# Kernel tuning notes

Measured on AMD Instinct MI355X. Metric: run time of the kernel, lower is better.

## Reference

```python
import jax, jax.numpy as jnp
import numpy as np

V, K, E, H, B, T = 30000, 9, 300, 300, 64, 512


def _lstm_dir(pre, W_hh, reverse):
    # pre: [T, B, 4H] = x @ W_ih.T + b_ih + b_hh, torch gate order (i, f, g, o)
    Bsz = pre.shape[1]
    Hh = W_hh.shape[1]
    h0 = jnp.zeros((Bsz, Hh), pre.dtype)
    c0 = jnp.zeros((Bsz, Hh), pre.dtype)

    def step(carry, p):
        h, c = carry
        gates = p + h @ W_hh.T
        i, f, g, o = jnp.split(gates, 4, axis=-1)
        i = jax.nn.sigmoid(i)
        f = jax.nn.sigmoid(f)
        o = jax.nn.sigmoid(o)
        g = jnp.tanh(g)
        c = f * c + i * g
        h = o * jnp.tanh(c)
        return (h, c), h

    _, hs = jax.lax.scan(step, (h0, c0), pre, reverse=reverse)
    return hs  # [T, B, H], time-aligned with input (reverse dir handled by scan)


def _crf_loglik(em, tags, mask, start, end, trans):
    # torchcrf CRF log-likelihood, reduction='sum'. em: [B,T,K], mask: [B,T] float.
    em_sc = jnp.take_along_axis(em, tags[..., None], axis=-1)[..., 0]  # [B,T]
    tr_sc = trans[tags[:, :-1], tags[:, 1:]]                            # [B,T-1]
    seq_len = jnp.sum(mask, axis=1).astype(jnp.int32)                   # [B]
    last_tags = jnp.take_along_axis(tags, (seq_len - 1)[:, None], axis=1)[:, 0]
    num = start[tags[:, 0]] + em_sc[:, 0]
    num = num + jnp.sum((tr_sc + em_sc[:, 1:]) * mask[:, 1:], axis=1)
    num = num + end[last_tags]

    # forward algorithm (partition function)
    alpha0 = start[None, :] + em[:, 0]             # [B,K]
    em_t = jnp.swapaxes(em[:, 1:], 0, 1)           # [T-1,B,K]
    m_t = jnp.swapaxes(mask[:, 1:], 0, 1)          # [T-1,B]

    def step(alpha, xs):
        e, m = xs
        nxt = jax.nn.logsumexp(alpha[:, :, None] + trans[None] + e[:, None, :], axis=1)
        return jnp.where(m[:, None] > 0, nxt, alpha), None

    alpha, _ = jax.lax.scan(step, alpha0, (em_t, m_t))
    den = jax.nn.logsumexp(alpha + end[None, :], axis=1)
    return jnp.sum(num - den)


def _forward(x, y, embedding, W_ih_f, W_hh_f, b_ih_f, b_hh_f,
             W_ih_b, W_hh_b, b_ih_b, b_hh_b, W_lin, b_lin,
             start_trans, end_trans, trans):
    emb = embedding[x]                       # [B,T,E]
    emb_t = jnp.swapaxes(emb, 0, 1)          # [T,B,E]
    pre_f = emb_t @ W_ih_f.T + (b_ih_f + b_hh_f)
    pre_b = emb_t @ W_ih_b.T + (b_ih_b + b_hh_b)
    hs_f = _lstm_dir(pre_f, W_hh_f, reverse=False)
    hs_b = _lstm_dir(pre_b, W_hh_b, reverse=True)
    out = jnp.concatenate([hs_f, hs_b], axis=-1)  # [T,B,2H]
    out = jnp.swapaxes(out, 0, 1)                 # [B,T,2H]
    logits = out @ W_lin.T + b_lin
    probs = jax.nn.softmax(logits, axis=-1)
    mask = (y != -1).astype(probs.dtype)
    llh = _crf_loglik(probs, y, mask, start_trans, end_trans, trans)
    return probs, -llh


def setup_inputs() -> dict:
    key = jax.random.key(0)
    ks = jax.random.split(key, 17)

    def p(k, shape, s=0.05):
        return jax.random.normal(k, shape, dtype=jnp.float32) * s

    return {
        "x": jax.random.randint(ks[0], (B, T), 0, V),
        "y": jax.random.randint(ks[1], (B, T), 0, K),
        "embedding": p(ks[2], (V, E), 1.0),
        "W_ih_f": p(ks[3], (4 * H, E)),
        "W_hh_f": p(ks[4], (4 * H, H)),
        "b_ih_f": p(ks[5], (4 * H,)),
        "b_hh_f": p(ks[6], (4 * H,)),
        "W_ih_b": p(ks[7], (4 * H, E)),
        "W_hh_b": p(ks[8], (4 * H, H)),
        "b_ih_b": p(ks[9], (4 * H,)),
        "b_hh_b": p(ks[10], (4 * H,)),
        "W_lin": p(ks[11], (K, 2 * H)),
        "b_lin": p(ks[12], (K,)),
        "start_trans": p(ks[13], (K,), 0.1),
        "end_trans": p(ks[14], (K,), 0.1),
        "trans": p(ks[15], (K, K), 0.1),
    }


def reference(x, y, embedding, W_ih_f, W_hh_f, b_ih_f, b_hh_f,
              W_ih_b, W_hh_b, b_ih_b, b_hh_b, W_lin, b_lin,
              start_trans, end_trans, trans):
    return _forward(x, y, embedding, W_ih_f, W_hh_f, b_ih_f, b_hh_f,
                    W_ih_b, W_hh_b, b_ih_b, b_hh_b, W_lin, b_lin,
                    start_trans, end_trans, trans)
```

## Files before the change

kernel.cpp:

```cpp
#include <hip/hip_runtime.h>
#include <stdint.h>

#define TSEQ 512
#define NB   64
#define EMB  300
#define HID  300
#define G4   1200
#define KKP  150
#define NT   9
#define MTOT (TSEQ*NB)

#define NP 19
#define NQ 4
#define NWG (2*NQ*NP)
#define KSTEPS 10
#define HROWS 160

typedef _Float16 h2v __attribute__((ext_vector_type(2)));
typedef _Float16 f16x8 __attribute__((ext_vector_type(8)));
typedef float f32x4 __attribute__((ext_vector_type(4)));
union H2U { uint32_t u; h2v h; };

__device__ __forceinline__ uint32_t packf2(float a, float b) {
  H2U u; u.h.x = (_Float16)a; u.h.y = (_Float16)b; return u.u;
}

__device__ __forceinline__ float sigm(float x) { return 1.0f / (1.0f + expf(-x)); }

__global__ __launch_bounds__(256) void prep_wih(
    const float* __restrict__ Wihf, const float* __restrict__ Wihb,
    uint32_t* __restrict__ wtih) {
  int i = blockIdx.x * 256 + threadIdx.x;
  if (i >= KKP * G4) return;
  int m = blockIdx.y;
  int kk = i / G4, g = i % G4;
  const float* src = (m == 0) ? Wihf : Wihb;
  float2 v = *(const float2*)(src + (size_t)g * 300 + 2 * kk);
  wtih[(size_t)m * (KKP * G4) + i] = packf2(v.x, v.y);
}

__global__ __launch_bounds__(256) void prep_bias(
    const float* __restrict__ bihf, const float* __restrict__ bhhf,
    const float* __restrict__ bihb, const float* __restrict__ bhhb,
    float* __restrict__ bias) {
  int i = blockIdx.x * 256 + threadIdx.x;
  if (i < G4) {
    bias[i]       = bihf[i] + bhhf[i];
    bias[G4 + i]  = bihb[i] + bhhb[i];
  }
}

__global__ __launch_bounds__(64) void prep_w3(
    const float* __restrict__ Whhf, const float* __restrict__ Whhb,
    uint32_t* __restrict__ w2) {
  int blk = blockIdx.x;
  int ks = blk % KSTEPS; int tmp = blk / KSTEPS;
  int w = tmp & 3; tmp >>= 2;
  int p = tmp % NP; int d = tmp / NP;
  int lane = threadIdx.x;
  const float* W = d ? Whhb : Whhf;
  int m = lane & 15;
  int gamma = m >> 2, rr = m & 3;
  int hid = 16 * p + 4 * w + rr;
  int k0 = ks * 32 + (lane >> 4) * 8;
  float vals[8];
  #pragma unroll
  for (int e = 0; e < 8; ++e) {
    int k = k0 + e;
    vals[e] = (hid < 300 && k < 300) ? W[(size_t)(gamma * 300 + hid) * 300 + k] : 0.0f;
  }
  uint4 dw;
  dw.x = packf2(vals[0], vals[1]);
  dw.y = packf2(vals[2], vals[3]);
  dw.z = packf2(vals[4], vals[5]);
  dw.w = packf2(vals[6], vals[7]);
  *(uint4*)(w2 + ((size_t)blk * 64 + lane) * 4) = dw;
}

__global__ __launch_bounds__(256) void init_sync(
    uint32_t* __restrict__ flags, uint32_t* __restrict__ h2g) {
  int i = blockIdx.x * 256 + threadIdx.x;
  if (i < 8 * 128) flags[i] = 0;
  if (i < 2 * 2 * HROWS * 64) h2g[i] = 0;
}

__global__ __launch_bounds__(256) void gather_emb(
    const int* __restrict__ x, const float* __restrict__ emb,
    uint32_t* __restrict__ Ae) {
  __shared__ __align__(16) uint32_t buf[64 * KKP];
  __shared__ int idxs[64];
  int tid = threadIdx.x;
  int m0 = blockIdx.x * 64;
  if (tid < 64) {
    int mm = m0 + tid;
    idxs[tid] = x[(size_t)(mm & 63) * TSEQ + (mm >> 6)];
  }
  __syncthreads();
  for (int i = tid; i < 64 * KKP; i += 256) {
    int mm = i / KKP, kk = i % KKP;
    float2 v = *(const float2*)(emb + (size_t)idxs[mm] * EMB + 2 * kk);
    buf[i] = packf2(v.x, v.y);
  }
  __syncthreads();
  for (int i = tid; i < 64 * KKP; i += 256) {
    int kk = i >> 6, mm = i & 63;
    Ae[(size_t)kk * MTOT + m0 + mm] = buf[mm * KKP + kk];
  }
}

__global__ __launch_bounds__(256) void embed_pre_mfma(
    const uint32_t* __restrict__ Ae, const uint32_t* __restrict__ wtih,
    const float* __restrict__ bias, _Float16* __restrict__ pre) {
  const int d = blockIdx.z;
  const int tid = threadIdx.x;
  const int w = tid >> 6, lane = tid & 63;
  const int n0 = blockIdx.x * 64 + w * 16;
  const int m00 = blockIdx.y * 128;
  const int col = n0 + (lane & 15);
  const bool colok = col < G4;
  const int rsel = lane >> 4;
  const uint32_t* Wd = wtih + (size_t)d * (KKP * G4);
  uint32_t bfr[KSTEPS][4];
  #pragma unroll
  for (int ks = 0; ks < KSTEPS; ++ks)
    #pragma unroll
    for (int j = 0; j < 4; ++j) {
      int kk = ks * 16 + rsel * 4 + j;
      bfr[ks][j] = (kk < KKP && colok) ? Wd[(size_t)kk * G4 + col] : 0u;
    }
  float bcol = colok ? bias[d * G4 + col] : 0.0f;
  for (int mb = 0; mb < 8; ++mb) {
    const int m0 = m00 + mb * 16;
    uint32_t afr[KSTEPS][4];
    #pragma unroll
    for (int ks = 0; ks < KSTEPS; ++ks)
      #pragma unroll
      for (int j = 0; j < 4; ++j) {
        int kk = ks * 16 + rsel * 4 + j;
        afr[ks][j] = (kk < KKP) ? Ae[(size_t)kk * MTOT + m0 + (lane & 15)] : 0u;
      }
    f32x4 acc; acc[0] = bcol; acc[1] = bcol; acc[2] = bcol; acc[3] = bcol;
    #pragma unroll
    for (int ks = 0; ks < KSTEPS; ++ks) {
      union { uint32_t u[4]; f16x8 v; } au, bu;
      au.u[0] = afr[ks][0]; au.u[1] = afr[ks][1]; au.u[2] = afr[ks][2]; au.u[3] = afr[ks][3];
      bu.u[0] = bfr[ks][0]; bu.u[1] = bfr[ks][1]; bu.u[2] = bfr[ks][2]; bu.u[3] = bfr[ks][3];
      acc = __builtin_amdgcn_mfma_f32_16x16x32_f16(au.v, bu.v, acc, 0, 0, 0);
    }
    if (colok) {
      #pragma unroll
      for (int j = 0; j < 4; ++j) {
        int m = m0 + rsel * 4 + j;
        pre[((size_t)d * MTOT + m) * G4 + col] = (_Float16)acc[j];
      }
    }
  }
}

__global__ __launch_bounds__(256) void lstm_mfma(
    const uint32_t* __restrict__ w2, const _Float16* __restrict__ pre,
    uint32_t* __restrict__ h2g, uint32_t* __restrict__ hs16,
    uint32_t* __restrict__ flags) {
  const int wg = blockIdx.x;
  const int p  = wg % NP;
  const int dq = wg / NP;
  const int q  = dq & 3;
  const int d  = dq >> 2;
  const int tid = threadIdx.x;
  const int w = tid >> 6;
  const int lane = tid & 63;
  const int G = lane >> 4;
  const int b = lane & 15;
  const int hidbase = 16 * p + 4 * w;
  const bool valid = hidbase < 300;

  __shared__ float xch[4 * 256];

  uint4 afr[KSTEPS];
  const int blk0 = ((d * NP + p) * 4 + w) * KSTEPS;
  #pragma unroll
  for (int ks = 0; ks < KSTEPS; ++ks)
    afr[ks] = *(const uint4*)(w2 + (size_t)(blk0 + ks) * 256 + (size_t)lane * 4);

  uint32_t* flagbase = flags + dq * 128;
  uint32_t* myflag = flagbase + p * 4 + w;
  float cstate = 0.0f;

  for (int s = 0; s < TSEQ; ++s) {
    const int t = d ? (TSEQ - 1 - s) : s;

    uint2 pr = make_uint2(0u, 0u);
    if (valid)
      pr = *(const uint2*)(pre + ((size_t)d * MTOT + (size_t)t * NB + 16 * q + b) * G4
                           + (G * 300 + hidbase));

    if (s > 0) {
      const uint32_t sv = (uint32_t)s;
      for (;;) {
        uint32_t v0 = __hip_atomic_load(flagbase + lane, __ATOMIC_RELAXED,
                                        __HIP_MEMORY_SCOPE_AGENT);
        uint32_t v1 = sv;
        if (lane < 12)
          v1 = __hip_atomic_load(flagbase + 64 + lane, __ATOMIC_RELAXED,
                                 __HIP_MEMORY_SCOPE_AGENT);
        if (__all((int)(v0 >= sv && v1 >= sv))) break;
      }
      asm volatile("" ::: "memory");
    }

    const uint32_t* hb = h2g + (size_t)(((s + 1) & 1) * 2 + d) * (HROWS * 64)
                         + 16 * q + b;
    uint32_t bf[KSTEPS][4];
    #pragma unroll
    for (int ks = 0; ks < KSTEPS; ++ks)
      #pragma unroll
      for (int j = 0; j < 4; ++j)
        bf[ks][j] = __hip_atomic_load(hb + (size_t)(ks * 16 + G * 4 + j) * 64,
                                      __ATOMIC_RELAXED, __HIP_MEMORY_SCOPE_AGENT);

    f32x4 acc0, acc1;
    {
      union { uint2 u; _Float16 h[4]; } cv; cv.u = pr;
      acc0[0] = (float)cv.h[0]; acc0[1] = (float)cv.h[1];
      acc0[2] = (float)cv.h[2]; acc0[3] = (float)cv.h[3];
      acc1[0] = 0.f; acc1[1] = 0.f; acc1[2] = 0.f; acc1[3] = 0.f;
    }
    #pragma unroll
    for (int ks = 0; ks < KSTEPS; ks += 2) {
      union { uint4 u; f16x8 v; } au0, au1;
      union { uint32_t u[4]; f16x8 v; } bu0, bu1;
      au0.u = afr[ks]; au1.u = afr[ks + 1];
      bu0.u[0] = bf[ks][0]; bu0.u[1] = bf[ks][1]; bu0.u[2] = bf[ks][2]; bu0.u[3] = bf[ks][3];
      bu1.u[0] = bf[ks+1][0]; bu1.u[1] = bf[ks+1][1]; bu1.u[2] = bf[ks+1][2]; bu1.u[3] = bf[ks+1][3];
      acc0 = __builtin_amdgcn_mfma_f32_16x16x32_f16(au0.v, bu0.v, acc0, 0, 0, 0);
      acc1 = __builtin_amdgcn_mfma_f32_16x16x32_f16(au1.v, bu1.v, acc1, 0, 0, 0);
    }
    #pragma unroll
    for (int j = 0; j < 4; ++j)
      xch[w * 256 + (j * 4 + G) * 16 + b] = acc0[j] + acc1[j];
    asm volatile("s_waitcnt lgkmcnt(0)" ::: "memory");
    float gi = xch[w * 256 + (G * 4 + 0) * 16 + b];
    float gf = xch[w * 256 + (G * 4 + 1) * 16 + b];
    float gg = xch[w * 256 + (G * 4 + 2) * 16 + b];
    float go = xch[w * 256 + (G * 4 + 3) * 16 + b];

    float iv = sigm(gi), fv = sigm(gf), gv = tanhf(gg), ov = sigm(go);
    cstate = fv * cstate + iv * gv;
    float h = ov * tanhf(cstate);

    float hp = __shfl_xor(h, 16);
    if (valid && (G & 1) == 0) {
      uint32_t dw = packf2(h, hp);
      int kk = (hidbase + G) >> 1;
      uint32_t* dst = h2g + (size_t)((s & 1) * 2 + d) * (HROWS * 64)
                      + (size_t)kk * 64 + 16 * q + b;
      __hip_atomic_store(dst, dw, __ATOMIC_RELAXED, __HIP_MEMORY_SCOPE_AGENT);
      hs16[((size_t)d * MTOT + (size_t)t * NB + 16 * q + b) * 152 + kk] = dw;
    }
    asm volatile("s_waitcnt vmcnt(0)" ::: "memory");
    if (lane == 0)
      __hip_atomic_store(myflag, (uint32_t)(s + 1), __ATOMIC_RELAXED,
                         __HIP_MEMORY_SCOPE_AGENT);
  }
}

__global__ __launch_bounds__(256) void logits_probs(
    const uint32_t* __restrict__ hs16, const float* __restrict__ Wlin,
    const float* __restrict__ blin, float* __restrict__ probs) {
  __shared__ float Ws[NT * 600];
  __shared__ float bs[NT];
  int tid = threadIdx.x;
  for (int i = tid; i < NT * 600; i += 256) Ws[i] = Wlin[i];
  if (tid < NT) bs[tid] = blin[tid];
  __syncthreads();
  int wave = tid >> 6, lane = tid & 63;
  for (int it = 0; it < 4; ++it) {
    int tb = blockIdx.x * 16 + wave * 4 + it;
    const uint32_t* hf = hs16 + (size_t)tb * 152;
    const uint32_t* hb = hs16 + ((size_t)MTOT + tb) * 152;
    uint32_t f0 = hf[lane], f1 = hf[64 + lane];
    uint32_t f2 = (lane < 22) ? hf[128 + lane] : 0u;
    uint32_t g0 = hb[lane], g1 = hb[64 + lane];
    uint32_t g2 = (lane < 22) ? hb[128 + lane] : 0u;
    float p[NT];
    #pragma unroll
    for (int k = 0; k < NT; ++k) p[k] = 0.f;
    uint32_t fa[3] = {f0, f1, f2};
    uint32_t ga[3] = {g0, g1, g2};
    #pragma unroll
    for (int c = 0; c < 3; ++c) {
      int kk = c * 64 + lane;
      if (kk < KKP) {
        H2U uf; uf.u = fa[c];
        H2U ug; ug.u = ga[c];
        float hf0 = (float)uf.h.x, hf1 = (float)uf.h.y;
        float hb0 = (float)ug.h.x, hb1 = (float)ug.h.y;
        #pragma unroll
        for (int k = 0; k < NT; ++k)
          p[k] += hf0 * Ws[k * 600 + 2 * kk] + hf1 * Ws[k * 600 + 2 * kk + 1]
                + hb0 * Ws[k * 600 + 300 + 2 * kk] + hb1 * Ws[k * 600 + 300 + 2 * kk + 1];
      }
    }
    #pragma unroll
    for (int off = 32; off > 0; off >>= 1)
      #pragma unroll
      for (int k = 0; k < NT; ++k) p[k] += __shfl_xor(p[k], off);
    float l[NT]; float mx = -1e30f;
    #pragma unroll
    for (int k = 0; k < NT; ++k) { l[k] = p[k] + bs[k]; mx = fmaxf(mx, l[k]); }
    float ssum = 0.f;
    #pragma unroll
    for (int k = 0; k < NT; ++k) ssum += expf(l[k] - mx);
    int t = tb >> 6, bb = tb & 63;
    if (lane < NT)
      probs[((size_t)bb * TSEQ + t) * NT + lane] = expf(l[lane] - mx) / ssum;
  }
}

__global__ __launch_bounds__(256) void crf_num(
    const int* __restrict__ y, const float* __restrict__ probs,
    const float* __restrict__ strt, const float* __restrict__ endt,
    const float* __restrict__ trans, float* __restrict__ nums) {
  int b = blockIdx.x, tid = threadIdx.x;
  __shared__ float r1[256], r2[256];
  float s = 0.f, cnt = 0.f;
  for (int t = tid; t < TSEQ; t += 256) {
    int yc = y[(size_t)b * TSEQ + t];
    cnt += (yc != -1) ? 1.f : 0.f;
    if (t >= 1) {
      int yp = y[(size_t)b * TSEQ + t - 1];
      float mask = (yc != -1) ? 1.f : 0.f;
      s += mask * (trans[yp * NT + yc] + probs[((size_t)b * TSEQ + t) * NT + yc]);
    }
  }
  r1[tid] = s; r2[tid] = cnt;
  __syncthreads();
  for (int off = 128; off > 0; off >>= 1) {
    if (tid < off) { r1[tid] += r1[tid + off]; r2[tid] += r2[tid + off]; }
    __syncthreads();
  }
  if (tid == 0) {
    int y0 = y[(size_t)b * TSEQ];
    int seqlen = (int)(r2[0] + 0.5f);
    int ylast = y[(size_t)b * TSEQ + seqlen - 1];
    nums[b] = strt[y0] + probs[((size_t)b * TSEQ) * NT + y0] + r1[0] + endt[ylast];
  }
}

__global__ __launch_bounds__(64) void crf_alpha(
    const int* __restrict__ y, const float* __restrict__ probs,
    const float* __restrict__ strt, const float* __restrict__ endt,
    const float* __restrict__ trans, float* __restrict__ dens) {
  int b = blockIdx.x, lane = threadIdx.x;
  __shared__ float P[TSEQ * NT];
  __shared__ float msk[TSEQ];
  for (int i = lane; i < TSEQ * NT; i += 64) P[i] = probs[(size_t)b * TSEQ * NT + i];
  for (int i = lane; i < TSEQ; i += 64) msk[i] = (y[(size_t)b * TSEQ + i] != -1) ? 1.f : 0.f;
  asm volatile("s_waitcnt lgkmcnt(0) vmcnt(0)" ::: "memory");
  int li = lane < NT ? lane : NT - 1;
  float trc[NT];
  #pragma unroll
  for (int j = 0; j < NT; ++j) trc[j] = trans[j * NT + li];
  float al = strt[li] + P[li];
  for (int t = 1; t < TSEQ; ++t) {
    float e = P[t * NT + li];
    float m = msk[t];
    float tmp[NT]; float mx = -1e30f;
    #pragma unroll
    for (int j = 0; j < NT; ++j) {
      float aj = __shfl(al, j);
      tmp[j] = aj + trc[j];
      mx = fmaxf(mx, tmp[j]);
    }
    float sum = 0.f;
    #pragma unroll
    for (int j = 0; j < NT; ++j) sum += expf(tmp[j] - mx);
    float nxt = e + mx + logf(sum);
    al = (m > 0.5f) ? nxt : al;
  }
  float v = al + endt[li];
  float mx = -1e30f;
  #pragma unroll
  for (int j = 0; j < NT; ++j) mx = fmaxf(mx, __shfl(v, j));
  float sum = 0.f;
  #pragma unroll
  for (int j = 0; j < NT; ++j) sum += expf(__shfl(v, j) - mx);
  if (lane == 0) dens[b] = mx + logf(sum);
}

__global__ __launch_bounds__(64) void final_sum(
    const float* __restrict__ nums, const float* __restrict__ dens,
    float* __restrict__ out) {
  __shared__ float r[64];
  int tid = threadIdx.x;
  r[tid] = nums[tid] - dens[tid];
  __syncthreads();
  for (int off = 32; off > 0; off >>= 1) {
    if (tid < off) r[tid] += r[tid + off];
    __syncthreads();
  }
  if (tid == 0) out[(size_t)MTOT * NT] = -r[0];
}

extern "C" void kernel_launch(void* const* d_in, const int* in_sizes, int n_in,
                              void* d_out, int out_size, void* d_ws, size_t ws_size,
                              hipStream_t stream) {
  (void)in_sizes; (void)n_in; (void)out_size;
  const int*   x     = (const int*)d_in[0];
  const int*   y     = (const int*)d_in[1];
  const float* emb   = (const float*)d_in[2];
  const float* Wihf  = (const float*)d_in[3];
  const float* Whhf  = (const float*)d_in[4];
  const float* bihf  = (const float*)d_in[5];
  const float* bhhf  = (const float*)d_in[6];
  const float* Wihb  = (const float*)d_in[7];
  const float* Whhb  = (const float*)d_in[8];
  const float* bihb  = (const float*)d_in[9];
  const float* bhhb  = (const float*)d_in[10];
  const float* Wlin  = (const float*)d_in[11];
  const float* blin  = (const float*)d_in[12];
  const float* strt  = (const float*)d_in[13];
  const float* endt  = (const float*)d_in[14];
  const float* trans = (const float*)d_in[15];
  float* outp = (float*)d_out;

  char* ws = (char*)d_ws;
  const size_t OFF_WTIH  = 0;
  const size_t OFF_W2    = 1440000;
  const size_t OFF_BIAS  = 2996480;
  const size_t OFF_NUMS  = 3006080;
  const size_t OFF_DENS  = 3006336;
  const size_t OFF_FLAGS = 3006592;
  const size_t OFF_H2G   = 3010688;
  const size_t OFF_AE    = 3174528;
  const size_t OFF_HS16  = 22835328;
  const size_t OFF_PRE   = 62681216;
  if (ws_size < 219967616ull) return;

  uint32_t* wtih  = (uint32_t*)(ws + OFF_WTIH);
  uint32_t* w2    = (uint32_t*)(ws + OFF_W2);
  float*    bias  = (float*)(ws + OFF_BIAS);
  float*    nums  = (float*)(ws + OFF_NUMS);
  float*    dens  = (float*)(ws + OFF_DENS);
  uint32_t* flags = (uint32_t*)(ws + OFF_FLAGS);
  uint32_t* h2g   = (uint32_t*)(ws + OFF_H2G);
  uint32_t* Ae    = (uint32_t*)(ws + OFF_AE);
  uint32_t* hs16  = (uint32_t*)(ws + OFF_HS16);
  _Float16* pre   = (_Float16*)(ws + OFF_PRE);

  prep_wih<<<dim3((KKP * G4 + 255) / 256, 2), 256, 0, stream>>>(Wihf, Wihb, wtih);
  prep_bias<<<dim3((G4 + 255) / 256), 256, 0, stream>>>(bihf, bhhf, bihb, bhhb, bias);
  prep_w3<<<dim3(2 * NP * 4 * KSTEPS), 64, 0, stream>>>(Whhf, Whhb, w2);
  init_sync<<<dim3(160), 256, 0, stream>>>(flags, h2g);
  gather_emb<<<dim3(MTOT / 64), 256, 0, stream>>>(x, emb, Ae);
  embed_pre_mfma<<<dim3(19, MTOT / 128, 2), 256, 0, stream>>>(Ae, wtih, bias, pre);
  lstm_mfma<<<dim3(NWG), 256, 0, stream>>>(w2, pre, h2g, hs16, flags);
  logits_probs<<<dim3(MTOT / 16), 256, 0, stream>>>(hs16, Wlin, blin, outp);
  crf_num<<<dim3(NB), 256, 0, stream>>>(y, outp, strt, endt, trans, nums);
  crf_alpha<<<dim3(NB), 64, 0, stream>>>(y, outp, strt, endt, trans, dens);
  final_sum<<<1, 64, 0, stream>>>(nums, dens, outp);
}
```

Before: 2.004 ms.

## Restructure persistent LSTM to 5 partitions with sentinel-based data-flagged exchange

The recurrent LSTM kernel moves from 152 workgroups (19 hidden partitions, one 16-row tile per wave) to 40 workgroups (5 partitions of 60 hidden units, 4 tiles per wave). Separate flag counters are replaced by sentinel-valued h buffers. Each producer broadcasts its h slice to per-consumer copies, and consumers poll the data itself, then reset it to the sentinel and stage it in LDS for the MFMA B operand. Fast exp2/rcp approximations replace expf/tanhf in the gates. The aim is to cut the per-timestep synchronization latency and the number of participants in the cross-workgroup barrier, at the cost of more MFMA work per workgroup, redundant stores, and lower-precision activations.

```diff
diff --git a/kernel.cpp b/kernel.cpp
--- a/kernel.cpp
+++ b/kernel.cpp
@@ -10,22 +10,30 @@
 #define NT   9
 #define MTOT (TSEQ*NB)
 
-#define NP 19
+#define KSTEPS 10
+#define NP5 5
 #define NQ 4
-#define NWG (2*NQ*NP)
-#define KSTEPS 10
-#define HROWS 160
-
-typedef _Float16 h2v __attribute__((ext_vector_type(2)));
+#define NWG5 (2*NQ*NP5)
+#define CPW 2560
+#define LSTR 68
+#define SENT64 0xFFFFFFFFFFFFFFFFull
+
 typedef _Float16 f16x8 __attribute__((ext_vector_type(8)));
 typedef float f32x4 __attribute__((ext_vector_type(4)));
-union H2U { uint32_t u; h2v h; };
+union H2U { uint32_t u; _Float16 h[2]; };
 
 __device__ __forceinline__ uint32_t packf2(float a, float b) {
-  H2U u; u.h.x = (_Float16)a; u.h.y = (_Float16)b; return u.u;
-}
-
-__device__ __forceinline__ float sigm(float x) { return 1.0f / (1.0f + expf(-x)); }
+  H2U u; u.h[0] = (_Float16)a; u.h[1] = (_Float16)b; return u.u;
+}
+__device__ __forceinline__ float fexp(float x) {
+  return __builtin_amdgcn_exp2f(x * 1.44269504088896f);
+}
+__device__ __forceinline__ float sigm(float x) {
+  return __builtin_amdgcn_rcpf(1.0f + fexp(-x));
+}
+__device__ __forceinline__ float ftanh(float x) {
+  return 1.0f - 2.0f * __builtin_amdgcn_rcpf(fexp(2.0f * x) + 1.0f);
+}
 
 __global__ __launch_bounds__(256) void prep_wih(
     const float* __restrict__ Wihf, const float* __restrict__ Wihb,
@@ -50,24 +58,24 @@
   }
 }
 
-__global__ __launch_bounds__(64) void prep_w3(
+__global__ __launch_bounds__(64) void prep_w5(
     const float* __restrict__ Whhf, const float* __restrict__ Whhb,
     uint32_t* __restrict__ w2) {
   int blk = blockIdx.x;
   int ks = blk % KSTEPS; int tmp = blk / KSTEPS;
-  int w = tmp & 3; tmp >>= 2;
-  int p = tmp % NP; int d = tmp / NP;
+  int qd = tmp % 15; tmp /= 15;
+  int p = tmp % NP5; int d = tmp / NP5;
   int lane = threadIdx.x;
   const float* W = d ? Whhb : Whhf;
   int m = lane & 15;
   int gamma = m >> 2, rr = m & 3;
-  int hid = 16 * p + 4 * w + rr;
+  int hid = p * 60 + qd * 4 + rr;
   int k0 = ks * 32 + (lane >> 4) * 8;
   float vals[8];
   #pragma unroll
   for (int e = 0; e < 8; ++e) {
     int k = k0 + e;
-    vals[e] = (hid < 300 && k < 300) ? W[(size_t)(gamma * 300 + hid) * 300 + k] : 0.0f;
+    vals[e] = (k < 300) ? W[(size_t)(gamma * 300 + hid) * 300 + k] : 0.0f;
   }
   uint4 dw;
   dw.x = packf2(vals[0], vals[1]);
@@ -77,11 +85,9 @@
   *(uint4*)(w2 + ((size_t)blk * 64 + lane) * 4) = dw;
 }
 
-__global__ __launch_bounds__(256) void init_sync(
-    uint32_t* __restrict__ flags, uint32_t* __restrict__ h2g) {
+__global__ __launch_bounds__(256) void init_sent(uint32_t* __restrict__ h2c) {
   int i = blockIdx.x * 256 + threadIdx.x;
-  if (i < 8 * 128) flags[i] = 0;
-  if (i < 2 * 2 * HROWS * 64) h2g[i] = 0;
+  if (i < 2 * 8 * NP5 * CPW) h2c[i] = 0xFFFFFFFFu;
 }
 
 __global__ __launch_bounds__(256) void gather_emb(
@@ -157,110 +163,144 @@
   }
 }
 
-__global__ __launch_bounds__(256) void lstm_mfma(
+__global__ __launch_bounds__(256, 1) void lstm_sent(
     const uint32_t* __restrict__ w2, const _Float16* __restrict__ pre,
-    uint32_t* __restrict__ h2g, uint32_t* __restrict__ hs16,
-    uint32_t* __restrict__ flags) {
+    uint32_t* __restrict__ h2c, uint32_t* __restrict__ hs16) {
   const int wg = blockIdx.x;
-  const int p  = wg % NP;
-  const int dq = wg / NP;
+  const int p  = wg % NP5;
+  const int dq = wg / NP5;
   const int q  = dq & 3;
   const int d  = dq >> 2;
   const int tid = threadIdx.x;
-  const int w = tid >> 6;
-  const int lane = tid & 63;
-  const int G = lane >> 4;
-  const int b = lane & 15;
-  const int hidbase = 16 * p + 4 * w;
-  const bool valid = hidbase < 300;
-
-  __shared__ float xch[4 * 256];
-
-  uint4 afr[KSTEPS];
-  const int blk0 = ((d * NP + p) * 4 + w) * KSTEPS;
-  #pragma unroll
-  for (int ks = 0; ks < KSTEPS; ++ks)
-    afr[ks] = *(const uint4*)(w2 + (size_t)(blk0 + ks) * 256 + (size_t)lane * 4);
-
-  uint32_t* flagbase = flags + dq * 128;
-  uint32_t* myflag = flagbase + p * 4 + w;
-  float cstate = 0.0f;
+  const int w = tid >> 6, lane = tid & 63;
+  const int G = lane >> 4, b = lane & 15;
+
+  __shared__ __align__(16) uint32_t hstg[2][40 * LSTR];
+  __shared__ float xch[4][4][272];
+
+  uint64_t* h2c64 = (uint64_t*)h2c;
+
+  uint4 afr[4][KSTEPS];
+  #pragma unroll
+  for (int tt = 0; tt < 4; ++tt) {
+    int qd = w * 4 + tt;
+    #pragma unroll
+    for (int ks = 0; ks < KSTEPS; ++ks) {
+      if (qd < 15)
+        afr[tt][ks] = *(const uint4*)(w2 +
+            ((size_t)(((d * NP5 + p) * 15 + qd) * KSTEPS + ks) * 64 + lane) * 4);
+      else
+        afr[tt][ks] = make_uint4(0u, 0u, 0u, 0u);
+    }
+  }
+
+  uint32_t pollmask = 0;
+  #pragma unroll
+  for (int r = 0; r < 5; ++r) {
+    int slot = tid + 256 * r;
+    int dw0 = slot * 2;
+    int kk = ((dw0 >> 6) << 2) + (dw0 & 3);
+    if (kk < 150) pollmask |= (1u << r);
+  }
+
+  float cst[4] = {0.f, 0.f, 0.f, 0.f};
 
   for (int s = 0; s < TSEQ; ++s) {
     const int t = d ? (TSEQ - 1 - s) : s;
-
-    uint2 pr = make_uint2(0u, 0u);
-    if (valid)
-      pr = *(const uint2*)(pre + ((size_t)d * MTOT + (size_t)t * NB + 16 * q + b) * G4
-                           + (G * 300 + hidbase));
-
+    const int par = s & 1;
+    const int rpar = (s + 1) & 1;
+
+    uint2 pr[4];
+    #pragma unroll
+    for (int tt = 0; tt < 4; ++tt) {
+      int qd = w * 4 + tt;
+      pr[tt] = make_uint2(0u, 0u);
+      if (qd < 15)
+        pr[tt] = *(const uint2*)(pre +
+            ((size_t)d * MTOT + (size_t)t * NB + 16 * q + b) * G4 +
+            (G * 300 + p * 60 + qd * 4));
+    }
+
+    uint64_t v[5] = {0ull, 0ull, 0ull, 0ull, 0ull};
     if (s > 0) {
-      const uint32_t sv = (uint32_t)s;
-      for (;;) {
-        uint32_t v0 = __hip_atomic_load(flagbase + lane, __ATOMIC_RELAXED,
-                                        __HIP_MEMORY_SCOPE_AGENT);
-        uint32_t v1 = sv;
-        if (lane < 12)
-          v1 = __hip_atomic_load(flagbase + 64 + lane, __ATOMIC_RELAXED,
-                                 __HIP_MEMORY_SCOPE_AGENT);
-        if (__all((int)(v0 >= sv && v1 >= sv))) break;
-      }
-      asm volatile("" ::: "memory");
-    }
-
-    const uint32_t* hb = h2g + (size_t)(((s + 1) & 1) * 2 + d) * (HROWS * 64)
-                         + 16 * q + b;
-    uint32_t bf[KSTEPS][4];
-    #pragma unroll
-    for (int ks = 0; ks < KSTEPS; ++ks)
+      uint64_t* src64 = h2c64 + ((size_t)(rpar * 8 + dq) * NP5 + p) * (CPW / 2);
+      uint32_t pend = pollmask;
+      while (pend) {
+        #pragma unroll
+        for (int r = 0; r < 5; ++r) {
+          if (pend & (1u << r)) {
+            uint64_t x = __hip_atomic_load(src64 + tid + 256 * r,
+                                           __ATOMIC_RELAXED, __HIP_MEMORY_SCOPE_AGENT);
+            if (x != SENT64) { v[r] = x; pend &= ~(1u << r); }
+          }
+        }
+      }
+      #pragma unroll
+      for (int r = 0; r < 5; ++r)
+        if (pollmask & (1u << r))
+          __hip_atomic_store(src64 + tid + 256 * r, SENT64,
+                             __ATOMIC_RELAXED, __HIP_MEMORY_SCOPE_AGENT);
+    }
+    #pragma unroll
+    for (int r = 0; r < 5; ++r) {
+      int slot = tid + 256 * r;
+      int dw0 = slot * 2;
+      int kkq = dw0 >> 6, brr = dw0 & 63;
+      *(uint64_t*)&hstg[rpar][kkq * LSTR + brr] = v[r];
+    }
+    __syncthreads();
+
+    f32x4 acc[4];
+    #pragma unroll
+    for (int tt = 0; tt < 4; ++tt) {
+      H2U c0, c1; c0.u = pr[tt].x; c1.u = pr[tt].y;
+      acc[tt][0] = (float)c0.h[0]; acc[tt][1] = (float)c0.h[1];
+      acc[tt][2] = (float)c1.h[0]; acc[tt][3] = (float)c1.h[1];
+    }
+    #pragma unroll
+    for (int ks = 0; ks < KSTEPS; ++ks) {
+      union { uint4 u; f16x8 v; } bu;
+      bu.u = *(const uint4*)&hstg[rpar][(ks * 4 + G) * LSTR + b * 4];
+      #pragma unroll
+      for (int tt = 0; tt < 4; ++tt) {
+        union { uint4 u; f16x8 v; } au; au.u = afr[tt][ks];
+        acc[tt] = __builtin_amdgcn_mfma_f32_16x16x32_f16(au.v, bu.v, acc[tt], 0, 0, 0);
+      }
+    }
+
+    #pragma unroll
+    for (int tt = 0; tt < 4; ++tt)
       #pragma unroll
       for (int j = 0; j < 4; ++j)
-        bf[ks][j] = __hip_atomic_load(hb + (size_t)(ks * 16 + G * 4 + j) * 64,
-                                      __ATOMIC_RELAXED, __HIP_MEMORY_SCOPE_AGENT);
-
-    f32x4 acc0, acc1;
-    {
-      union { uint2 u; _Float16 h[4]; } cv; cv.u = pr;
-      acc0[0] = (float)cv.h[0]; acc0[1] = (float)cv.h[1];
-      acc0[2] = (float)cv.h[2]; acc0[3] = (float)cv.h[3];
-      acc1[0] = 0.f; acc1[1] = 0.f; acc1[2] = 0.f; acc1[3] = 0.f;
-    }
-    #pragma unroll
-    for (int ks = 0; ks < KSTEPS; ks += 2) {
-      union { uint4 u; f16x8 v; } au0, au1;
-      union { uint32_t u[4]; f16x8 v; } bu0, bu1;
-      au0.u = afr[ks]; au1.u = afr[ks + 1];
-      bu0.u[0] = bf[ks][0]; bu0.u[1] = bf[ks][1]; bu0.u[2] = bf[ks][2]; bu0.u[3] = bf[ks][3];
-      bu1.u[0] = bf[ks+1][0]; bu1.u[1] = bf[ks+1][1]; bu1.u[2] = bf[ks+1][2]; bu1.u[3] = bf[ks+1][3];
-      acc0 = __builtin_amdgcn_mfma_f32_16x16x32_f16(au0.v, bu0.v, acc0, 0, 0, 0);
-      acc1 = __builtin_amdgcn_mfma_f32_16x16x32_f16(au1.v, bu1.v, acc1, 0, 0, 0);
-    }
-    #pragma unroll
-    for (int j = 0; j < 4; ++j)
-      xch[w * 256 + (j * 4 + G) * 16 + b] = acc0[j] + acc1[j];
+        xch[w][tt][(j * 4 + G) * 17 + b] = acc[tt][j];
     asm volatile("s_waitcnt lgkmcnt(0)" ::: "memory");
-    float gi = xch[w * 256 + (G * 4 + 0) * 16 + b];
-    float gf = xch[w * 256 + (G * 4 + 1) * 16 + b];
-    float gg = xch[w * 256 + (G * 4 + 2) * 16 + b];
-    float go = xch[w * 256 + (G * 4 + 3) * 16 + b];
-
-    float iv = sigm(gi), fv = sigm(gf), gv = tanhf(gg), ov = sigm(go);
-    cstate = fv * cstate + iv * gv;
-    float h = ov * tanhf(cstate);
-
-    float hp = __shfl_xor(h, 16);
-    if (valid && (G & 1) == 0) {
+    __builtin_amdgcn_sched_barrier(0);
+
+    #pragma unroll
+    for (int tt = 0; tt < 4; ++tt) {
+      int qd = w * 4 + tt;
+      float gi = xch[w][tt][(G * 4 + 0) * 17 + b];
+      float gf = xch[w][tt][(G * 4 + 1) * 17 + b];
+      float gg = xch[w][tt][(G * 4 + 2) * 17 + b];
+      float go = xch[w][tt][(G * 4 + 3) * 17 + b];
+      float iv = sigm(gi), fv = sigm(gf), gv = ftanh(gg), ov = sigm(go);
+      float c = fv * cst[tt] + iv * gv; cst[tt] = c;
+      float h = ov * ftanh(c);
+      float hp = __shfl_xor(h, 16);
       uint32_t dw = packf2(h, hp);
-      int kk = (hidbase + G) >> 1;
-      uint32_t* dst = h2g + (size_t)((s & 1) * 2 + d) * (HROWS * 64)
-                      + (size_t)kk * 64 + 16 * q + b;
-      __hip_atomic_store(dst, dw, __ATOMIC_RELAXED, __HIP_MEMORY_SCOPE_AGENT);
-      hs16[((size_t)d * MTOT + (size_t)t * NB + 16 * q + b) * 152 + kk] = dw;
-    }
-    asm volatile("s_waitcnt vmcnt(0)" ::: "memory");
-    if (lane == 0)
-      __hip_atomic_store(myflag, (uint32_t)(s + 1), __ATOMIC_RELAXED,
-                         __HIP_MEMORY_SCOPE_AGENT);
+      uint32_t hi = __shfl_xor(dw, 32);
+      if (qd < 15 && G == 0) {
+        uint64_t val = (uint64_t)dw | ((uint64_t)hi << 32);
+        int kk = p * 30 + qd * 2;
+        int slot = (((kk >> 2) * 64) + b * 4 + (kk & 3)) >> 1;
+        uint64_t* dst = h2c64 + ((size_t)(par * 8 + dq) * NP5) * (CPW / 2) + slot;
+        #pragma unroll
+        for (int cp = 0; cp < NP5; ++cp)
+          __hip_atomic_store(dst + cp * (CPW / 2), val,
+                             __ATOMIC_RELAXED, __HIP_MEMORY_SCOPE_AGENT);
+        *(uint64_t*)(hs16 + ((size_t)d * MTOT + (size_t)t * NB + 16 * q + b) * 152 + kk) = val;
+      }
+    }
   }
 }
 
@@ -278,23 +318,22 @@
     int tb = blockIdx.x * 16 + wave * 4 + it;
     const uint32_t* hf = hs16 + (size_t)tb * 152;
     const uint32_t* hb = hs16 + ((size_t)MTOT + tb) * 152;
-    uint32_t f0 = hf[lane], f1 = hf[64 + lane];
-    uint32_t f2 = (lane < 22) ? hf[128 + lane] : 0u;
-    uint32_t g0 = hb[lane], g1 = hb[64 + lane];
-    uint32_t g2 = (lane < 22) ? hb[128 + lane] : 0u;
+    uint32_t fa[3], ga[3];
+    fa[0] = hf[lane]; fa[1] = hf[64 + lane];
+    fa[2] = (lane < 22) ? hf[128 + lane] : 0u;
+    ga[0] = hb[lane]; ga[1] = hb[64 + lane];
+    ga[2] = (lane < 22) ? hb[128 + lane] : 0u;
     float p[NT];
     #pragma unroll
     for (int k = 0; k < NT; ++k) p[k] = 0.f;
-    uint32_t fa[3] = {f0, f1, f2};
-    uint32_t ga[3] = {g0, g1, g2};
     #pragma unroll
     for (int c = 0; c < 3; ++c) {
       int kk = c * 64 + lane;
       if (kk < KKP) {
         H2U uf; uf.u = fa[c];
         H2U ug; ug.u = ga[c];
-        float hf0 = (float)uf.h.x, hf1 = (float)uf.h.y;
-        float hb0 = (float)ug.h.x, hb1 = (float)ug.h.y;
+        float hf0 = (float)uf.h[0], hf1 = (float)uf.h[1];
+        float hb0 = (float)ug.h[0], hb1 = (float)ug.h[1];
         #pragma unroll
         for (int k = 0; k < NT; ++k)
           p[k] += hf0 * Ws[k * 600 + 2 * kk] + hf1 * Ws[k * 600 + 2 * kk + 1]
@@ -378,13 +417,13 @@
     float nxt = e + mx + logf(sum);
     al = (m > 0.5f) ? nxt : al;
   }
-  float v = al + endt[li];
+  float vv = al + endt[li];
   float mx = -1e30f;
   #pragma unroll
-  for (int j = 0; j < NT; ++j) mx = fmaxf(mx, __shfl(v, j));
+  for (int j = 0; j < NT; ++j) mx = fmaxf(mx, __shfl(vv, j));
   float sum = 0.f;
   #pragma unroll
-  for (int j = 0; j < NT; ++j) sum += expf(__shfl(v, j) - mx);
+  for (int j = 0; j < NT; ++j) sum += expf(__shfl(vv, j) - mx);
   if (lane == 0) dens[b] = mx + logf(sum);
 }
 
@@ -425,36 +464,34 @@
   float* outp = (float*)d_out;
 
   char* ws = (char*)d_ws;
-  const size_t OFF_WTIH  = 0;
-  const size_t OFF_W2    = 1440000;
-  const size_t OFF_BIAS  = 2996480;
-  const size_t OFF_NUMS  = 3006080;
-  const size_t OFF_DENS  = 3006336;
-  const size_t OFF_FLAGS = 3006592;
-  const size_t OFF_H2G   = 3010688;
-  const size_t OFF_AE    = 3174528;
-  const size_t OFF_HS16  = 22835328;
-  const size_t OFF_PRE   = 62681216;
-  if (ws_size < 219967616ull) return;
-
-  uint32_t* wtih  = (uint32_t*)(ws + OFF_WTIH);
-  uint32_t* w2    = (uint32_t*)(ws + OFF_W2);
-  float*    bias  = (float*)(ws + OFF_BIAS);
-  float*    nums  = (float*)(ws + OFF_NUMS);
-  float*    dens  = (float*)(ws + OFF_DENS);
-  uint32_t* flags = (uint32_t*)(ws + OFF_FLAGS);
-  uint32_t* h2g   = (uint32_t*)(ws + OFF_H2G);
-  uint32_t* Ae    = (uint32_t*)(ws + OFF_AE);
-  uint32_t* hs16  = (uint32_t*)(ws + OFF_HS16);
-  _Float16* pre   = (_Float16*)(ws + OFF_PRE);
+  const size_t OFF_WTIH = 0;
+  const size_t OFF_W2   = 1440000;
+  const size_t OFF_BIAS = 2976000;
+  const size_t OFF_NUMS = 2985600;
+  const size_t OFF_DENS = 2985856;
+  const size_t OFF_H2C  = 2986112;
+  const size_t OFF_AE   = 3805312;
+  const size_t OFF_HS16 = 23466112;
+  const size_t OFF_PRE  = 63312000;
+  if (ws_size < 220598400ull) return;
+
+  uint32_t* wtih = (uint32_t*)(ws + OFF_WTIH);
+  uint32_t* w2   = (uint32_t*)(ws + OFF_W2);
+  float*    bias = (float*)(ws + OFF_BIAS);
+  float*    nums = (float*)(ws + OFF_NUMS);
+  float*    dens = (float*)(ws + OFF_DENS);
+  uint32_t* h2c  = (uint32_t*)(ws + OFF_H2C);
+  uint32_t* Ae   = (uint32_t*)(ws + OFF_AE);
+  uint32_t* hs16 = (uint32_t*)(ws + OFF_HS16);
+  _Float16* pre  = (_Float16*)(ws + OFF_PRE);
 
   prep_wih<<<dim3((KKP * G4 + 255) / 256, 2), 256, 0, stream>>>(Wihf, Wihb, wtih);
   prep_bias<<<dim3((G4 + 255) / 256), 256, 0, stream>>>(bihf, bhhf, bihb, bhhb, bias);
-  prep_w3<<<dim3(2 * NP * 4 * KSTEPS), 64, 0, stream>>>(Whhf, Whhb, w2);
-  init_sync<<<dim3(160), 256, 0, stream>>>(flags, h2g);
+  prep_w5<<<dim3(2 * NP5 * 15 * KSTEPS), 64, 0, stream>>>(Whhf, Whhb, w2);
+  init_sent<<<dim3((2 * 8 * NP5 * CPW + 255) / 256), 256, 0, stream>>>(h2c);
   gather_emb<<<dim3(MTOT / 64), 256, 0, stream>>>(x, emb, Ae);
   embed_pre_mfma<<<dim3(19, MTOT / 128, 2), 256, 0, stream>>>(Ae, wtih, bias, pre);
-  lstm_mfma<<<dim3(NWG), 256, 0, stream>>>(w2, pre, h2g, hs16, flags);
+  lstm_sent<<<dim3(NWG5), 256, 0, stream>>>(w2, pre, h2c, hs16);
   logits_probs<<<dim3(MTOT / 16), 256, 0, stream>>>(hs16, Wlin, blin, outp);
   crf_num<<<dim3(NB), 256, 0, stream>>>(y, outp, strt, endt, trans, nums);
   crf_alpha<<<dim3(NB), 64, 0, stream>>>(y, outp, strt, endt, trans, dens);
```

Result: slower. 2.647 ms (+32.1%).

## Fuse input projection into persistent LSTM kernel and use fast exp/tanh

Applied to the files above, without the earlier changes.

Removes the separate embedding-projection GEMM kernel and its large fp16 pre-activation buffer. The input projection is instead computed inside each recurrent step with extra MFMAs over register-resident W_ih fragments, reading embeddings from the gathered buffer, which has its padding rows zeroed. Sigmoid and tanh now use hardware exp2/rcp intrinsics. This adds per-step compute and loads to the latency-critical serial loop, and the fast intrinsics are slightly less accurate.

```diff
diff --git a/kernel.cpp b/kernel.cpp
--- a/kernel.cpp
+++ b/kernel.cpp
@@ -16,27 +16,21 @@
 #define KSTEPS 10
 #define HROWS 160
 
-typedef _Float16 h2v __attribute__((ext_vector_type(2)));
 typedef _Float16 f16x8 __attribute__((ext_vector_type(8)));
 typedef float f32x4 __attribute__((ext_vector_type(4)));
-union H2U { uint32_t u; h2v h; };
+union H2U { uint32_t u; _Float16 h[2]; };
 
 __device__ __forceinline__ uint32_t packf2(float a, float b) {
-  H2U u; u.h.x = (_Float16)a; u.h.y = (_Float16)b; return u.u;
-}
-
-__device__ __forceinline__ float sigm(float x) { return 1.0f / (1.0f + expf(-x)); }
-
-__global__ __launch_bounds__(256) void prep_wih(
-    const float* __restrict__ Wihf, const float* __restrict__ Wihb,
-    uint32_t* __restrict__ wtih) {
-  int i = blockIdx.x * 256 + threadIdx.x;
-  if (i >= KKP * G4) return;
-  int m = blockIdx.y;
-  int kk = i / G4, g = i % G4;
-  const float* src = (m == 0) ? Wihf : Wihb;
-  float2 v = *(const float2*)(src + (size_t)g * 300 + 2 * kk);
-  wtih[(size_t)m * (KKP * G4) + i] = packf2(v.x, v.y);
+  H2U u; u.h[0] = (_Float16)a; u.h[1] = (_Float16)b; return u.u;
+}
+__device__ __forceinline__ float fexp(float x) {
+  return __builtin_amdgcn_exp2f(x * 1.44269504088896f);
+}
+__device__ __forceinline__ float sigm(float x) {
+  return __builtin_amdgcn_rcpf(1.0f + fexp(-x));
+}
+__device__ __forceinline__ float ftanh(float x) {
+  return 1.0f - 2.0f * __builtin_amdgcn_rcpf(fexp(2.0f * x) + 1.0f);
 }
 
 __global__ __launch_bounds__(256) void prep_bias(
@@ -50,15 +44,17 @@
   }
 }
 
-__global__ __launch_bounds__(64) void prep_w3(
+__global__ __launch_bounds__(64) void prep_wf(
+    const float* __restrict__ Wihf, const float* __restrict__ Wihb,
     const float* __restrict__ Whhf, const float* __restrict__ Whhb,
-    uint32_t* __restrict__ w2) {
+    uint32_t* __restrict__ wf) {
   int blk = blockIdx.x;
   int ks = blk % KSTEPS; int tmp = blk / KSTEPS;
   int w = tmp & 3; tmp >>= 2;
-  int p = tmp % NP; int d = tmp / NP;
+  int p = tmp % NP; tmp /= NP;
+  int d = tmp & 1; int kind = tmp >> 1;
   int lane = threadIdx.x;
-  const float* W = d ? Whhb : Whhf;
+  const float* W = kind ? (d ? Whhb : Whhf) : (d ? Wihb : Wihf);
   int m = lane & 15;
   int gamma = m >> 2, rr = m & 3;
   int hid = 16 * p + 4 * w + rr;
@@ -74,7 +70,7 @@
   dw.y = packf2(vals[2], vals[3]);
   dw.z = packf2(vals[4], vals[5]);
   dw.w = packf2(vals[6], vals[7]);
-  *(uint4*)(w2 + ((size_t)blk * 64 + lane) * 4) = dw;
+  *(uint4*)(wf + ((size_t)blk * 64 + lane) * 4) = dw;
 }
 
 __global__ __launch_bounds__(256) void init_sync(
@@ -106,59 +102,15 @@
     int kk = i >> 6, mm = i & 63;
     Ae[(size_t)kk * MTOT + m0 + mm] = buf[mm * KKP + kk];
   }
-}
-
-__global__ __launch_bounds__(256) void embed_pre_mfma(
-    const uint32_t* __restrict__ Ae, const uint32_t* __restrict__ wtih,
-    const float* __restrict__ bias, _Float16* __restrict__ pre) {
-  const int d = blockIdx.z;
-  const int tid = threadIdx.x;
-  const int w = tid >> 6, lane = tid & 63;
-  const int n0 = blockIdx.x * 64 + w * 16;
-  const int m00 = blockIdx.y * 128;
-  const int col = n0 + (lane & 15);
-  const bool colok = col < G4;
-  const int rsel = lane >> 4;
-  const uint32_t* Wd = wtih + (size_t)d * (KKP * G4);
-  uint32_t bfr[KSTEPS][4];
-  #pragma unroll
-  for (int ks = 0; ks < KSTEPS; ++ks)
-    #pragma unroll
-    for (int j = 0; j < 4; ++j) {
-      int kk = ks * 16 + rsel * 4 + j;
-      bfr[ks][j] = (kk < KKP && colok) ? Wd[(size_t)kk * G4 + col] : 0u;
-    }
-  float bcol = colok ? bias[d * G4 + col] : 0.0f;
-  for (int mb = 0; mb < 8; ++mb) {
-    const int m0 = m00 + mb * 16;
-    uint32_t afr[KSTEPS][4];
-    #pragma unroll
-    for (int ks = 0; ks < KSTEPS; ++ks)
-      #pragma unroll
-      for (int j = 0; j < 4; ++j) {
-        int kk = ks * 16 + rsel * 4 + j;
-        afr[ks][j] = (kk < KKP) ? Ae[(size_t)kk * MTOT + m0 + (lane & 15)] : 0u;
-      }
-    f32x4 acc; acc[0] = bcol; acc[1] = bcol; acc[2] = bcol; acc[3] = bcol;
-    #pragma unroll
-    for (int ks = 0; ks < KSTEPS; ++ks) {
-      union { uint32_t u[4]; f16x8 v; } au, bu;
-      au.u[0] = afr[ks][0]; au.u[1] = afr[ks][1]; au.u[2] = afr[ks][2]; au.u[3] = afr[ks][3];
-      bu.u[0] = bfr[ks][0]; bu.u[1] = bfr[ks][1]; bu.u[2] = bfr[ks][2]; bu.u[3] = bfr[ks][3];
-      acc = __builtin_amdgcn_mfma_f32_16x16x32_f16(au.v, bu.v, acc, 0, 0, 0);
-    }
-    if (colok) {
-      #pragma unroll
-      for (int j = 0; j < 4; ++j) {
-        int m = m0 + rsel * 4 + j;
-        pre[((size_t)d * MTOT + m) * G4 + col] = (_Float16)acc[j];
-      }
-    }
-  }
-}
-
-__global__ __launch_bounds__(256) void lstm_mfma(
-    const uint32_t* __restrict__ w2, const _Float16* __restrict__ pre,
+  for (int i = tid; i < 64 * (HROWS - KKP); i += 256) {
+    int kk = KKP + (i >> 6), mm = i & 63;
+    Ae[(size_t)kk * MTOT + m0 + mm] = 0u;
+  }
+}
+
+__global__ __launch_bounds__(256, 1) void lstm_mfma(
+    const uint32_t* __restrict__ wf, const uint32_t* __restrict__ Ae,
+    const float* __restrict__ bias,
     uint32_t* __restrict__ h2g, uint32_t* __restrict__ hs16,
     uint32_t* __restrict__ flags) {
   const int wg = blockIdx.x;
@@ -173,14 +125,25 @@
   const int b = lane & 15;
   const int hidbase = 16 * p + 4 * w;
   const bool valid = hidbase < 300;
+  const int bglob = 16 * q + b;
 
   __shared__ float xch[4 * 256];
 
-  uint4 afr[KSTEPS];
-  const int blk0 = ((d * NP + p) * 4 + w) * KSTEPS;
+  uint4 ai[KSTEPS], ah[KSTEPS];
+  const int blkI = (((0 * 2 + d) * NP + p) * 4 + w) * KSTEPS;
+  const int blkH = (((1 * 2 + d) * NP + p) * 4 + w) * KSTEPS;
   #pragma unroll
-  for (int ks = 0; ks < KSTEPS; ++ks)
-    afr[ks] = *(const uint4*)(w2 + (size_t)(blk0 + ks) * 256 + (size_t)lane * 4);
+  for (int ks = 0; ks < KSTEPS; ++ks) {
+    ai[ks] = *(const uint4*)(wf + ((size_t)(blkI + ks) * 64 + lane) * 4);
+    ah[ks] = *(const uint4*)(wf + ((size_t)(blkH + ks) * 64 + lane) * 4);
+  }
+
+  float b4[4] = {0.f, 0.f, 0.f, 0.f};
+  if (valid) {
+    #pragma unroll
+    for (int j = 0; j < 4; ++j)
+      b4[j] = bias[d * G4 + G * 300 + hidbase + j];
+  }
 
   uint32_t* flagbase = flags + dq * 128;
   uint32_t* myflag = flagbase + p * 4 + w;
@@ -189,10 +152,15 @@
   for (int s = 0; s < TSEQ; ++s) {
     const int t = d ? (TSEQ - 1 - s) : s;
 
-    uint2 pr = make_uint2(0u, 0u);
-    if (valid)
-      pr = *(const uint2*)(pre + ((size_t)d * MTOT + (size_t)t * NB + 16 * q + b) * G4
-                           + (G * 300 + hidbase));
+    uint32_t ab[KSTEPS][4];
+    {
+      const uint32_t* asrc = Ae + (size_t)t * NB + bglob;
+      #pragma unroll
+      for (int ks = 0; ks < KSTEPS; ++ks)
+        #pragma unroll
+        for (int j = 0; j < 4; ++j)
+          ab[ks][j] = asrc[(size_t)(ks * 16 + G * 4 + j) * MTOT];
+    }
 
     if (s > 0) {
       const uint32_t sv = (uint32_t)s;
@@ -209,7 +177,7 @@
     }
 
     const uint32_t* hb = h2g + (size_t)(((s + 1) & 1) * 2 + d) * (HROWS * 64)
-                         + 16 * q + b;
+                         + bglob;
     uint32_t bf[KSTEPS][4];
     #pragma unroll
     for (int ks = 0; ks < KSTEPS; ++ks)
@@ -219,43 +187,43 @@
                                       __ATOMIC_RELAXED, __HIP_MEMORY_SCOPE_AGENT);
 
     f32x4 acc0, acc1;
-    {
-      union { uint2 u; _Float16 h[4]; } cv; cv.u = pr;
-      acc0[0] = (float)cv.h[0]; acc0[1] = (float)cv.h[1];
-      acc0[2] = (float)cv.h[2]; acc0[3] = (float)cv.h[3];
-      acc1[0] = 0.f; acc1[1] = 0.f; acc1[2] = 0.f; acc1[3] = 0.f;
-    }
-    #pragma unroll
-    for (int ks = 0; ks < KSTEPS; ks += 2) {
-      union { uint4 u; f16x8 v; } au0, au1;
-      union { uint32_t u[4]; f16x8 v; } bu0, bu1;
-      au0.u = afr[ks]; au1.u = afr[ks + 1];
-      bu0.u[0] = bf[ks][0]; bu0.u[1] = bf[ks][1]; bu0.u[2] = bf[ks][2]; bu0.u[3] = bf[ks][3];
-      bu1.u[0] = bf[ks+1][0]; bu1.u[1] = bf[ks+1][1]; bu1.u[2] = bf[ks+1][2]; bu1.u[3] = bf[ks+1][3];
-      acc0 = __builtin_amdgcn_mfma_f32_16x16x32_f16(au0.v, bu0.v, acc0, 0, 0, 0);
-      acc1 = __builtin_amdgcn_mfma_f32_16x16x32_f16(au1.v, bu1.v, acc1, 0, 0, 0);
-    }
+    acc0[0] = b4[0]; acc0[1] = b4[1]; acc0[2] = b4[2]; acc0[3] = b4[3];
+    acc1[0] = 0.f; acc1[1] = 0.f; acc1[2] = 0.f; acc1[3] = 0.f;
+    #pragma unroll
+    for (int ks = 0; ks < KSTEPS; ++ks) {
+      union { uint4 u; f16x8 v; } aiu, ahu;
+      union { uint32_t u[4]; f16x8 v; } abu, bfu;
+      aiu.u = ai[ks]; ahu.u = ah[ks];
+      abu.u[0] = ab[ks][0]; abu.u[1] = ab[ks][1];
+      abu.u[2] = ab[ks][2]; abu.u[3] = ab[ks][3];
+      bfu.u[0] = bf[ks][0]; bfu.u[1] = bf[ks][1];
+      bfu.u[2] = bf[ks][2]; bfu.u[3] = bf[ks][3];
+      acc0 = __builtin_amdgcn_mfma_f32_16x16x32_f16(aiu.v, abu.v, acc0, 0, 0, 0);
+      acc1 = __builtin_amdgcn_mfma_f32_16x16x32_f16(ahu.v, bfu.v, acc1, 0, 0, 0);
+    }
+
     #pragma unroll
     for (int j = 0; j < 4; ++j)
       xch[w * 256 + (j * 4 + G) * 16 + b] = acc0[j] + acc1[j];
     asm volatile("s_waitcnt lgkmcnt(0)" ::: "memory");
+    __builtin_amdgcn_sched_barrier(0);
     float gi = xch[w * 256 + (G * 4 + 0) * 16 + b];
     float gf = xch[w * 256 + (G * 4 + 1) * 16 + b];
     float gg = xch[w * 256 + (G * 4 + 2) * 16 + b];
     float go = xch[w * 256 + (G * 4 + 3) * 16 + b];
 
-    float iv = sigm(gi), fv = sigm(gf), gv = tanhf(gg), ov = sigm(go);
+    float iv = sigm(gi), fv = sigm(gf), gv = ftanh(gg), ov = sigm(go);
     cstate = fv * cstate + iv * gv;
-    float h = ov * tanhf(cstate);
+    float h = ov * ftanh(cstate);
 
     float hp = __shfl_xor(h, 16);
     if (valid && (G & 1) == 0) {
       uint32_t dw = packf2(h, hp);
       int kk = (hidbase + G) >> 1;
       uint32_t* dst = h2g + (size_t)((s & 1) * 2 + d) * (HROWS * 64)
-                      + (size_t)kk * 64 + 16 * q + b;
+                      + (size_t)kk * 64 + bglob;
       __hip_atomic_store(dst, dw, __ATOMIC_RELAXED, __HIP_MEMORY_SCOPE_AGENT);
-      hs16[((size_t)d * MTOT + (size_t)t * NB + 16 * q + b) * 152 + kk] = dw;
+      hs16[((size_t)d * MTOT + (size_t)t * NB + bglob) * 152 + kk] = dw;
     }
     asm volatile("s_waitcnt vmcnt(0)" ::: "memory");
     if (lane == 0)
@@ -278,23 +246,22 @@
     int tb = blockIdx.x * 16 + wave * 4 + it;
     const uint32_t* hf = hs16 + (size_t)tb * 152;
     const uint32_t* hb = hs16 + ((size_t)MTOT + tb) * 152;
-    uint32_t f0 = hf[lane], f1 = hf[64 + lane];
-    uint32_t f2 = (lane < 22) ? hf[128 + lane] : 0u;
-    uint32_t g0 = hb[lane], g1 = hb[64 + lane];
-    uint32_t g2 = (lane < 22) ? hb[128 + lane] : 0u;
+    uint32_t fa[3], ga[3];
+    fa[0] = hf[lane]; fa[1] = hf[64 + lane];
+    fa[2] = (lane < 22) ? hf[128 + lane] : 0u;
+    ga[0] = hb[lane]; ga[1] = hb[64 + lane];
+    ga[2] = (lane < 22) ? hb[128 + lane] : 0u;
     float p[NT];
     #pragma unroll
     for (int k = 0; k < NT; ++k) p[k] = 0.f;
-    uint32_t fa[3] = {f0, f1, f2};
-    uint32_t ga[3] = {g0, g1, g2};
     #pragma unroll
     for (int c = 0; c < 3; ++c) {
       int kk = c * 64 + lane;
       if (kk < KKP) {
         H2U uf; uf.u = fa[c];
         H2U ug; ug.u = ga[c];
-        float hf0 = (float)uf.h.x, hf1 = (float)uf.h.y;
-        float hb0 = (float)ug.h.x, hb1 = (float)ug.h.y;
+        float hf0 = (float)uf.h[0], hf1 = (float)uf.h[1];
+        float hb0 = (float)ug.h[0], hb1 = (float)ug.h[1];
         #pragma unroll
         for (int k = 0; k < NT; ++k)
           p[k] += hf0 * Ws[k * 600 + 2 * kk] + hf1 * Ws[k * 600 + 2 * kk + 1]
@@ -378,13 +345,13 @@
     float nxt = e + mx + logf(sum);
     al = (m > 0.5f) ? nxt : al;
   }
-  float v = al + endt[li];
+  float vv = al + endt[li];
   float mx = -1e30f;
   #pragma unroll
-  for (int j = 0; j < NT; ++j) mx = fmaxf(mx, __shfl(v, j));
+  for (int j = 0; j < NT; ++j) mx = fmaxf(mx, __shfl(vv, j));
   float sum = 0.f;
   #pragma unroll
-  for (int j = 0; j < NT; ++j) sum += expf(__shfl(v, j) - mx);
+  for (int j = 0; j < NT; ++j) sum += expf(__shfl(vv, j) - mx);
   if (lane == 0) dens[b] = mx + logf(sum);
 }
 
@@ -425,20 +392,17 @@
   float* outp = (float*)d_out;
 
   char* ws = (char*)d_ws;
-  const size_t OFF_WTIH  = 0;
-  const size_t OFF_W2    = 1440000;
-  const size_t OFF_BIAS  = 2996480;
-  const size_t OFF_NUMS  = 3006080;
-  const size_t OFF_DENS  = 3006336;
-  const size_t OFF_FLAGS = 3006592;
-  const size_t OFF_H2G   = 3010688;
-  const size_t OFF_AE    = 3174528;
-  const size_t OFF_HS16  = 22835328;
-  const size_t OFF_PRE   = 62681216;
-  if (ws_size < 219967616ull) return;
-
-  uint32_t* wtih  = (uint32_t*)(ws + OFF_WTIH);
-  uint32_t* w2    = (uint32_t*)(ws + OFF_W2);
+  const size_t OFF_WF    = 0;
+  const size_t OFF_BIAS  = 3112960;
+  const size_t OFF_NUMS  = 3122560;
+  const size_t OFF_DENS  = 3122816;
+  const size_t OFF_FLAGS = 3123072;
+  const size_t OFF_H2G   = 3127168;
+  const size_t OFF_AE    = 3291008;
+  const size_t OFF_HS16  = 24262528;
+  if (ws_size < 64108416ull) return;
+
+  uint32_t* wf    = (uint32_t*)(ws + OFF_WF);
   float*    bias  = (float*)(ws + OFF_BIAS);
   float*    nums  = (float*)(ws + OFF_NUMS);
   float*    dens  = (float*)(ws + OFF_DENS);
@@ -446,15 +410,12 @@
   uint32_t* h2g   = (uint32_t*)(ws + OFF_H2G);
   uint32_t* Ae    = (uint32_t*)(ws + OFF_AE);
   uint32_t* hs16  = (uint32_t*)(ws + OFF_HS16);
-  _Float16* pre   = (_Float16*)(ws + OFF_PRE);
-
-  prep_wih<<<dim3((KKP * G4 + 255) / 256, 2), 256, 0, stream>>>(Wihf, Wihb, wtih);
+
+  prep_wf<<<dim3(2 * 2 * NP * 4 * KSTEPS), 64, 0, stream>>>(Wihf, Wihb, Whhf, Whhb, wf);
   prep_bias<<<dim3((G4 + 255) / 256), 256, 0, stream>>>(bihf, bhhf, bihb, bhhb, bias);
-  prep_w3<<<dim3(2 * NP * 4 * KSTEPS), 64, 0, stream>>>(Whhf, Whhb, w2);
   init_sync<<<dim3(160), 256, 0, stream>>>(flags, h2g);
   gather_emb<<<dim3(MTOT / 64), 256, 0, stream>>>(x, emb, Ae);
-  embed_pre_mfma<<<dim3(19, MTOT / 128, 2), 256, 0, stream>>>(Ae, wtih, bias, pre);
-  lstm_mfma<<<dim3(NWG), 256, 0, stream>>>(w2, pre, h2g, hs16, flags);
+  lstm_mfma<<<dim3(NWG), 256, 0, stream>>>(wf, Ae, bias, h2g, hs16, flags);
   logits_probs<<<dim3(MTOT / 16), 256, 0, stream>>>(hs16, Wlin, blin, outp);
   crf_num<<<dim3(NB), 256, 0, stream>>>(y, outp, strt, endt, trans, nums);
   crf_alpha<<<dim3(NB), 64, 0, stream>>>(y, outp, strt, endt, trans, dens);
```

Result: faster. 1.832 ms (-8.6%).
